# Kernel optimization log

Measured on AMD Instinct MI355X. Metric: run time of the kernel, lower is better.

Reference implementation:

```python
import jax, jax.numpy as jnp
import numpy as np

N_NODES, N_RELS, D, DEG = 100000, 2000, 128, 16
N_EDGES = N_NODES * DEG


def setup_inputs() -> dict:
    key = jax.random.key(0)
    k1, k2, k3, k4, k5 = jax.random.split(key, 5)
    # subject column: sorted and covers every node (tf.math.segment_sum requires
    # sorted segment ids; full coverage avoids 0/0 in the normalization)
    subj = jnp.repeat(jnp.arange(N_NODES, dtype=jnp.int64), DEG)
    rel = jax.random.randint(k1, (N_EDGES,), 0, N_RELS, dtype=jnp.int64)
    obj = jax.random.randint(k2, (N_EDGES,), 0, N_NODES, dtype=jnp.int64)
    triples = jnp.stack([subj, rel, obj], axis=1)[None]  # [1, E, 3]
    features = jax.random.normal(k3, (N_NODES, D), jnp.float32)
    rel_emb = jax.random.normal(k4, (N_RELS, D), jnp.float32)
    attn_kernel = jax.random.normal(k5, (D, 1), jnp.float32) * 0.05  # keep exp() finite
    return {"triples": triples, "features": features, "rel_emb": rel_emb,
            "attn_kernel": attn_kernel}


def reference(triples, features, rel_emb, attn_kernel):
    # single head, 'concat' reduction, linear activation, no bias
    t = jnp.squeeze(triples, 0).astype(jnp.int32)  # [E, 3]
    subj, rel_idx, obj_idx = t[:, 0], t[:, 1], t[:, 2]
    n = features.shape[0]

    obj_embs = features[obj_idx]          # [E, D] gather
    edge_embs = rel_emb[rel_idx]          # [E, D] gather

    # tf.nn.l2_normalize(edge_embs, 1) with eps 1e-12
    edge_n = edge_embs * jax.lax.rsqrt(
        jnp.maximum(jnp.sum(edge_embs * edge_embs, axis=1, keepdims=True), 1e-12))
    # Householder-like reflection (note: projection onto normalized dir, scaled
    # by the UNnormalized edge embedding, exactly as in the source)
    refl = jnp.sum(obj_embs * edge_n, axis=1, keepdims=True) * edge_embs
    obj_embs = obj_embs - 2.0 * refl      # [E, D]

    # per-relation attention logit, gathered per edge
    att_value = jnp.exp(rel_emb @ attn_kernel)[rel_idx]  # [E, 1]

    num = jax.ops.segment_sum(att_value * obj_embs, subj, num_segments=n)  # [N, D]
    den = jax.ops.segment_sum(att_value, subj, num_segments=n)             # [N, 1]
    return num / den
```

## Files before the change

### kernel.cpp

```cpp
#include <hip/hip_runtime.h>
#include <hip/hip_fp16.h>

#define N_NODES 100000
#define N_RELS  2000
#define D       128
#define DEG     16

#define RELWS_BYTES  16384
#define FEAT16_BYTES ((size_t)N_NODES * D * 2)
#define REL16_BYTES  ((size_t)N_RELS * D * 2)
#define WS_NEED      (RELWS_BYTES + FEAT16_BYTES + REL16_BYTES)

static __device__ __forceinline__ __half2 bc_h2(unsigned int u) {
  return __builtin_bit_cast(__half2, u);
}
static __device__ __forceinline__ int bc_i(float f) {
  return __builtin_bit_cast(int, f);
}
static __device__ __forceinline__ float bc_f(int i) {
  return __builtin_bit_cast(float, i);
}

static __device__ __forceinline__ float row16_sum_bcast(float v) {
  v += bc_f(__builtin_amdgcn_update_dpp(0, bc_i(v), 0x111, 0xF, 0xF, false));
  v += bc_f(__builtin_amdgcn_update_dpp(0, bc_i(v), 0x112, 0xF, 0xF, false));
  v += bc_f(__builtin_amdgcn_update_dpp(0, bc_i(v), 0x114, 0xF, 0xF, false));
  v += bc_f(__builtin_amdgcn_update_dpp(0, bc_i(v), 0x118, 0xF, 0xF, false));
  return bc_f(__builtin_amdgcn_ds_swizzle(bc_i(v), 0x1F0));
}

__global__ __launch_bounds__(256) void rel_pre_kernel(
    const float* __restrict__ rel_emb,
    const float* __restrict__ attn,
    float2* __restrict__ relws,
    unsigned int* __restrict__ rel16u) {
  const int wave = threadIdx.x >> 6;
  const int lane = threadIdx.x & 63;
  const int r = blockIdx.x * 4 + wave;
  float2 ev = *(const float2*)(rel_emb + (size_t)r * D + lane * 2);
  float2 av = *(const float2*)(attn + lane * 2);
  rel16u[r * 64 + lane] =
      __builtin_bit_cast(unsigned int, __builtin_amdgcn_cvt_pkrtz(ev.x, ev.y));
  float ss = ev.x * ev.x + ev.y * ev.y;
  float dt = ev.x * av.x + ev.y * av.y;
#pragma unroll
  for (int off = 32; off >= 1; off >>= 1) {
    ss += __shfl_xor(ss, off, 64);
    dt += __shfl_xor(dt, off, 64);
  }
  if (lane == 0) {
    float inv = rsqrtf(fmaxf(ss, 1e-12f));
    relws[r] = make_float2(inv, expf(dt));
  }
}

__global__ __launch_bounds__(256) void cvt_f32_f16_kernel(
    const float* __restrict__ src, uint2* __restrict__ dst) {
  const int i = blockIdx.x * 256 + threadIdx.x;
  float4 v = ((const float4*)src)[i];
  uint2 o;
  o.x = __builtin_bit_cast(unsigned int, __builtin_amdgcn_cvt_pkrtz(v.x, v.y));
  o.y = __builtin_bit_cast(unsigned int, __builtin_amdgcn_cvt_pkrtz(v.z, v.w));
  dst[i] = o;
}

__global__ __launch_bounds__(256) void gat16_kernel(
    const int* __restrict__ triples,
    const unsigned short* __restrict__ feat16,
    const unsigned short* __restrict__ rel16,
    const float2* __restrict__ relws,
    float* __restrict__ out) {
  __shared__ uint2 recs[256];

  const int tid  = threadIdx.x;
  const int s    = tid & 15;
  const int g    = (tid >> 4) & 3;
  const int wave = tid >> 6;
  const int node = blockIdx.x * 16 + wave * 4 + g;

  const int* t = triples + (size_t)node * (DEG * 3);
  const int tr = t[3 * s + 1];
  const int to = t[3 * s + 2];
  const float2 ia = relws[tr];
  const float att = ia.y;
  const float cf  = 2.f * att * ia.x;

  float den = att;
  den += __shfl_xor(den, 1);
  den += __shfl_xor(den, 2);
  den += __shfl_xor(den, 4);
  den += __shfl_xor(den, 8);
  const float rden = 1.f / den;

  recs[tid] = make_uint2(
      (unsigned int)((to << 11) | tr),
      __builtin_bit_cast(unsigned int, __builtin_amdgcn_cvt_pkrtz(att, cf)));
  __syncthreads();

  const int rbase = tid & 0xF0;

  uint4 ofb[8], efb[8];
  unsigned int pacb[8];
#pragma unroll
  for (int i = 0; i < 8; ++i) {
    uint2 r = recs[rbase + i];
    pacb[i] = r.y;
    ofb[i] = *(const uint4*)(feat16 + (size_t)(r.x >> 11) * D + s * 8);
    efb[i] = *(const uint4*)(rel16 + (size_t)(r.x & 2047u) * D + s * 8);
  }

  __half2 acc1[4], acc2[4];
#pragma unroll
  for (int j = 0; j < 4; ++j) {
    acc1[j] = __float2half2_rn(0.f);
    acc2[j] = __float2half2_rn(0.f);
  }

#pragma unroll
  for (int i = 0; i < DEG; ++i) {
    const int j = i & 7;
    const uint4 of = ofb[j];
    const uint4 ef = efb[j];
    const unsigned int ac = pacb[j];
    if (i + 8 < DEG) {
      uint2 r = recs[rbase + i + 8];
      pacb[j] = r.y;
      ofb[j] = *(const uint4*)(feat16 + (size_t)(r.x >> 11) * D + s * 8);
      efb[j] = *(const uint4*)(rel16 + (size_t)(r.x & 2047u) * D + s * 8);
    }

    const __half2 o0 = bc_h2(of.x), o1 = bc_h2(of.y), o2 = bc_h2(of.z), o3 = bc_h2(of.w);
    const __half2 e0 = bc_h2(ef.x), e1 = bc_h2(ef.y), e2 = bc_h2(ef.z), e3 = bc_h2(ef.w);

    __half2 pp = __hmul2(o0, e0);
    pp = __hfma2(o1, e1, pp);
    pp = __hfma2(o2, e2, pp);
    pp = __hfma2(o3, e3, pp);
    const float pd = row16_sum_bcast(__low2float(pp) + __high2float(pp));

    const __half2 h = bc_h2(ac);
    const __half2 att2 = __half2half2(__low2half(h));
    const __half2 c2 = __float2half2_rn(__high2float(h) * pd);

    acc1[0] = __hfma2(att2, o0, acc1[0]);
    acc1[1] = __hfma2(att2, o1, acc1[1]);
    acc1[2] = __hfma2(att2, o2, acc1[2]);
    acc1[3] = __hfma2(att2, o3, acc1[3]);
    acc2[0] = __hfma2(c2, e0, acc2[0]);
    acc2[1] = __hfma2(c2, e1, acc2[1]);
    acc2[2] = __hfma2(c2, e2, acc2[2]);
    acc2[3] = __hfma2(c2, e3, acc2[3]);
  }

  float* op = out + (size_t)node * D + s * 8;
  float4 r0, r1;
  {
    float2 a0 = __half22float2(acc1[0]), b0 = __half22float2(acc2[0]);
    float2 a1 = __half22float2(acc1[1]), b1 = __half22float2(acc2[1]);
    r0.x = (a0.x - b0.x) * rden; r0.y = (a0.y - b0.y) * rden;
    r0.z = (a1.x - b1.x) * rden; r0.w = (a1.y - b1.y) * rden;
    float2 a2 = __half22float2(acc1[2]), b2 = __half22float2(acc2[2]);
    float2 a3 = __half22float2(acc1[3]), b3 = __half22float2(acc2[3]);
    r1.x = (a2.x - b2.x) * rden; r1.y = (a2.y - b2.y) * rden;
    r1.z = (a3.x - b3.x) * rden; r1.w = (a3.y - b3.y) * rden;
  }
  *(float4*)op = r0;
  *(float4*)(op + 4) = r1;
}

__global__ __launch_bounds__(256) void gat_kernel(
    const int* __restrict__ triples,
    const float* __restrict__ features,
    const float* __restrict__ rel_emb,
    const float2* __restrict__ relws,
    float* __restrict__ out) {
  const int wave = threadIdx.x >> 6;
  const int lane = threadIdx.x & 63;
  const int node = blockIdx.x * 4 + wave;
  const int* t = triples + (size_t)node * DEG * 3;
  int tv = (lane < DEG * 3) ? t[lane] : 0;
  float2 acc = make_float2(0.f, 0.f);
  float den = 0.f;
#pragma unroll
  for (int i = 0; i < DEG; ++i) {
    const int rel = __builtin_amdgcn_readfirstlane(__shfl(tv, 3 * i + 1, 64));
    const int obj = __builtin_amdgcn_readfirstlane(__shfl(tv, 3 * i + 2, 64));
    float2 ia = relws[rel];
    float2 ov = *(const float2*)(features + (size_t)obj * D + lane * 2);
    float2 ev = *(const float2*)(rel_emb + (size_t)rel * D + lane * 2);
    float pd = ov.x * ev.x + ov.y * ev.y;
#pragma unroll
    for (int off = 32; off >= 1; off >>= 1) pd += __shfl_xor(pd, off, 64);
    const float c = 2.f * pd * ia.x;
    const float att = ia.y;
    acc.x += att * (ov.x - c * ev.x);
    acc.y += att * (ov.y - c * ev.y);
    den += att;
  }
  const float r = 1.f / den;
  *(float2*)(out + (size_t)node * D + lane * 2) =
      make_float2(acc.x * r, acc.y * r);
}

extern "C" void kernel_launch(void* const* d_in, const int* in_sizes, int n_in,
                              void* d_out, int out_size, void* d_ws, size_t ws_size,
                              hipStream_t stream) {
  const int*   triples  = (const int*)d_in[0];
  const float* features = (const float*)d_in[1];
  const float* rel_emb  = (const float*)d_in[2];
  const float* attn     = (const float*)d_in[3];
  float*       out      = (float*)d_out;

  float2* relws = (float2*)d_ws;

  if (ws_size >= WS_NEED) {
    unsigned short* feat16 = (unsigned short*)((char*)d_ws + RELWS_BYTES);
    unsigned int*   rel16u = (unsigned int*)((char*)d_ws + RELWS_BYTES + FEAT16_BYTES);
    rel_pre_kernel<<<N_RELS / 4, 256, 0, stream>>>(rel_emb, attn, relws, rel16u);
    cvt_f32_f16_kernel<<<(N_NODES * D / 4) / 256, 256, 0, stream>>>(
        features, (uint2*)feat16);
    gat16_kernel<<<N_NODES / 16, 256, 0, stream>>>(
        triples, feat16, (const unsigned short*)rel16u, relws, out);
  } else {
    rel_pre_kernel<<<N_RELS / 4, 256, 0, stream>>>(rel_emb, attn, relws,
                                                   (unsigned int*)d_ws);
    gat_kernel<<<N_NODES / 4, 256, 0, stream>>>(
        triples, features, rel_emb, relws, out);
  }
}
```

Baseline: 173.9 us.

## Batch DPP reductions across edges and broadcast edge records via shuffles

Removes the shared-memory record staging and barrier, broadcasting packed edge indices and coefficients with wave shuffles instead. The per-edge 16-lane dot-product reduction is split out of the main loop so all 16 partial sums are reduced together, interleaving independent DPP chains to hide their latency. The relation rows are loaded a second time in a separate pass to apply the reflection term, which adds memory traffic and register pressure in exchange for shorter dependency chains.

```diff
diff --git a/kernel.cpp b/kernel.cpp
--- a/kernel.cpp
+++ b/kernel.cpp
@@ -21,12 +21,9 @@
   return __builtin_bit_cast(float, i);
 }
 
-static __device__ __forceinline__ float row16_sum_bcast(float v) {
-  v += bc_f(__builtin_amdgcn_update_dpp(0, bc_i(v), 0x111, 0xF, 0xF, false));
-  v += bc_f(__builtin_amdgcn_update_dpp(0, bc_i(v), 0x112, 0xF, 0xF, false));
-  v += bc_f(__builtin_amdgcn_update_dpp(0, bc_i(v), 0x114, 0xF, 0xF, false));
-  v += bc_f(__builtin_amdgcn_update_dpp(0, bc_i(v), 0x118, 0xF, 0xF, false));
-  return bc_f(__builtin_amdgcn_ds_swizzle(bc_i(v), 0x1F0));
+template <int CTRL>
+static __device__ __forceinline__ float dpp_add(float v) {
+  return v + bc_f(__builtin_amdgcn_update_dpp(0, bc_i(v), CTRL, 0xF, 0xF, false));
 }
 
 __global__ __launch_bounds__(256) void rel_pre_kernel(
@@ -70,8 +67,6 @@
     const unsigned short* __restrict__ rel16,
     const float2* __restrict__ relws,
     float* __restrict__ out) {
-  __shared__ uint2 recs[256];
-
   const int tid  = threadIdx.x;
   const int s    = tid & 15;
   const int g    = (tid >> 4) & 3;
@@ -92,43 +87,26 @@
   den += __shfl_xor(den, 8);
   const float rden = 1.f / den;
 
-  recs[tid] = make_uint2(
-      (unsigned int)((to << 11) | tr),
-      __builtin_bit_cast(unsigned int, __builtin_amdgcn_cvt_pkrtz(att, cf)));
-  __syncthreads();
-
-  const int rbase = tid & 0xF0;
-
-  uint4 ofb[8], efb[8];
-  unsigned int pacb[8];
-#pragma unroll
-  for (int i = 0; i < 8; ++i) {
-    uint2 r = recs[rbase + i];
-    pacb[i] = r.y;
-    ofb[i] = *(const uint4*)(feat16 + (size_t)(r.x >> 11) * D + s * 8);
-    efb[i] = *(const uint4*)(rel16 + (size_t)(r.x & 2047u) * D + s * 8);
-  }
-
-  __half2 acc1[4], acc2[4];
-#pragma unroll
-  for (int j = 0; j < 4; ++j) {
-    acc1[j] = __float2half2_rn(0.f);
-    acc2[j] = __float2half2_rn(0.f);
-  }
-
-#pragma unroll
-  for (int i = 0; i < DEG; ++i) {
-    const int j = i & 7;
-    const uint4 of = ofb[j];
-    const uint4 ef = efb[j];
-    const unsigned int ac = pacb[j];
-    if (i + 8 < DEG) {
-      uint2 r = recs[rbase + i + 8];
-      pacb[j] = r.y;
-      ofb[j] = *(const uint4*)(feat16 + (size_t)(r.x >> 11) * D + s * 8);
-      efb[j] = *(const uint4*)(rel16 + (size_t)(r.x & 2047u) * D + s * 8);
-    }
-
+  const int pidx = (to << 11) | tr;
+  const int pattcf =
+      __builtin_bit_cast(int, __builtin_amdgcn_cvt_pkrtz(att, cf));
+  const int srcBase = tid & 48;
+  int pb[DEG], ab[DEG];
+#pragma unroll
+  for (int i = 0; i < DEG; ++i) {
+    pb[i] = __shfl(pidx, srcBase + i, 64);
+    ab[i] = __shfl(pattcf, srcBase + i, 64);
+  }
+
+  float pd[DEG];
+  __half2 acc1[4];
+#pragma unroll
+  for (int j = 0; j < 4; ++j) acc1[j] = __float2half2_rn(0.f);
+
+#pragma unroll
+  for (int i = 0; i < DEG; ++i) {
+    const uint4 of = *(const uint4*)(feat16 + (size_t)(pb[i] >> 11) * D + s * 8);
+    const uint4 ef = *(const uint4*)(rel16 + (size_t)(pb[i] & 2047) * D + s * 8);
     const __half2 o0 = bc_h2(of.x), o1 = bc_h2(of.y), o2 = bc_h2(of.z), o3 = bc_h2(of.w);
     const __half2 e0 = bc_h2(ef.x), e1 = bc_h2(ef.y), e2 = bc_h2(ef.z), e3 = bc_h2(ef.w);
 
@@ -136,20 +114,41 @@
     pp = __hfma2(o1, e1, pp);
     pp = __hfma2(o2, e2, pp);
     pp = __hfma2(o3, e3, pp);
-    const float pd = row16_sum_bcast(__low2float(pp) + __high2float(pp));
-
-    const __half2 h = bc_h2(ac);
-    const __half2 att2 = __half2half2(__low2half(h));
-    const __half2 c2 = __float2half2_rn(__high2float(h) * pd);
-
+    pd[i] = __low2float(pp) + __high2float(pp);
+
+    const __half2 att2 = __half2half2(__low2half(bc_h2((unsigned int)ab[i])));
     acc1[0] = __hfma2(att2, o0, acc1[0]);
     acc1[1] = __hfma2(att2, o1, acc1[1]);
     acc1[2] = __hfma2(att2, o2, acc1[2]);
     acc1[3] = __hfma2(att2, o3, acc1[3]);
-    acc2[0] = __hfma2(c2, e0, acc2[0]);
-    acc2[1] = __hfma2(c2, e1, acc2[1]);
-    acc2[2] = __hfma2(c2, e2, acc2[2]);
-    acc2[3] = __hfma2(c2, e3, acc2[3]);
+  }
+
+#pragma unroll
+  for (int i = 0; i < DEG; ++i) pd[i] = dpp_add<0x111>(pd[i]);
+#pragma unroll
+  for (int i = 0; i < DEG; ++i) pd[i] = dpp_add<0x112>(pd[i]);
+#pragma unroll
+  for (int i = 0; i < DEG; ++i) pd[i] = dpp_add<0x114>(pd[i]);
+#pragma unroll
+  for (int i = 0; i < DEG; ++i) pd[i] = dpp_add<0x118>(pd[i]);
+#pragma unroll
+  for (int i = 0; i < DEG; ++i) {
+    pd[i] = bc_f(__builtin_amdgcn_ds_swizzle(bc_i(pd[i]), 0x1F0));
+  }
+
+  __half2 acc2[4];
+#pragma unroll
+  for (int j = 0; j < 4; ++j) acc2[j] = __float2half2_rn(0.f);
+
+#pragma unroll
+  for (int i = 0; i < DEG; ++i) {
+    const uint4 ef = *(const uint4*)(rel16 + (size_t)(pb[i] & 2047) * D + s * 8);
+    const float c = __high2float(bc_h2((unsigned int)ab[i])) * pd[i];
+    const __half2 c2 = __float2half2_rn(c);
+    acc2[0] = __hfma2(c2, bc_h2(ef.x), acc2[0]);
+    acc2[1] = __hfma2(c2, bc_h2(ef.y), acc2[1]);
+    acc2[2] = __hfma2(c2, bc_h2(ef.z), acc2[2]);
+    acc2[3] = __hfma2(c2, bc_h2(ef.w), acc2[3]);
   }
 
   float* op = out + (size_t)node * D + s * 8;
```

Measured after the change: 175.4 us. Within noise of the previous version (+0.9%).
